# Performance work log

Measured on AMD Instinct MI355X. Metric: run time of the kernel, lower is better.

## Reference

```python
import jax, jax.numpy as jnp
import numpy as np
from jax import lax

N_QUBITS = 12
N_LAYERS = 5
DIM = 2 ** N_QUBITS
EPS = 1e-5


def _linear(x, W, b):
    return x @ W.T + b


def _bn(x, g, b):
    # BatchNorm1d in training mode: biased batch statistics
    mu = jnp.mean(x, axis=0)
    var = jnp.var(x, axis=0)
    return g * (x - mu) * lax.rsqrt(var + EPS) + b


def _leaky(x):
    return jax.nn.leaky_relu(x, 0.01)


def _gate_matrices(w):
    # w: (L, Q, 3) -> composite U3 @ RZ @ RY @ RX per (layer, qubit): (L, Q, 2, 2) complex64
    a, b, c = w[..., 0], w[..., 1], w[..., 2]
    ca = jnp.cos(a / 2).astype(jnp.complex64)
    sa = jnp.sin(a / 2).astype(jnp.complex64)
    cb = jnp.cos(b / 2).astype(jnp.complex64)
    sb = jnp.sin(b / 2).astype(jnp.complex64)
    zero = jnp.zeros_like(ca)

    def mat(m00, m01, m10, m11):
        return jnp.stack([jnp.stack([m00, m01], -1), jnp.stack([m10, m11], -1)], -2)

    RX = mat(ca, -1j * sa, -1j * sa, ca)
    RY = mat(cb, -sb, sb, cb)
    ez = jnp.exp(-0.5j * c.astype(jnp.complex64))
    RZ = mat(ez, zero, zero, jnp.conj(ez))
    eip = jnp.exp(1j * b.astype(jnp.complex64))
    eid = jnp.exp(1j * c.astype(jnp.complex64))
    U3 = mat(ca, -eid * sa, eip * sa, eip * eid * ca)  # pennylane U3(theta=a, phi=b, delta=c)
    mm = lambda A, B: jnp.einsum('lqab,lqbc->lqac', A, B)
    return mm(U3, mm(RZ, mm(RY, RX)))


def _apply1q(state, U, w):
    # state: (B, 2, ..., 2); U: (2, 2) shared across batch
    s = jnp.moveaxis(state, 1 + w, -1)
    s = jnp.einsum('...a,ca->...c', s, U)
    return jnp.moveaxis(s, -1, 1 + w)


def _cnot(state, c, t):
    s = jnp.moveaxis(state, (1 + c, 1 + t), (-2, -1))
    s = jnp.stack([s[..., 0, :], s[..., 1, ::-1]], axis=-2)
    return jnp.moveaxis(s, (-2, -1), (1 + c, 1 + t))


def _quantum(x_pre, qw):
    # Batched statevector simulation of the pennylane circuit. x_pre: (B, 12)
    B = x_pre.shape[0]
    half = x_pre * (jnp.pi / 2)  # RY(x*pi) from |0> -> [cos(x*pi/2), sin(x*pi/2)]
    vec = jnp.stack([jnp.cos(half), jnp.sin(half)], axis=-1).astype(jnp.complex64)  # (B, Q, 2)
    state = vec[:, 0]
    for q in range(1, N_QUBITS):
        state = jnp.einsum('b...,bq->b...q', state, vec[:, q])  # (B, 2, ..., 2)
    G = _gate_matrices(qw)
    for l in range(N_LAYERS):
        for q in range(N_QUBITS):
            state = _apply1q(state, G[l, q], q)
        if l % 2 == 0:
            for q in range(N_QUBITS - 1):
                state = _cnot(state, q, q + 1)
            state = _cnot(state, N_QUBITS - 1, 0)
        else:
            for q in range(0, N_QUBITS, 2):
                state = _cnot(state, q, (q + N_QUBITS // 2) % N_QUBITS)
    probs = jnp.abs(state.reshape(B, DIM)) ** 2
    idx = np.arange(DIM)
    bits = (idx[None, :] >> (N_QUBITS - 1 - np.arange(N_QUBITS))[:, None]) & 1  # (Q, DIM)
    zsigns = jnp.asarray(1.0 - 2.0 * bits, dtype=jnp.float32)
    zvals = probs @ zsigns.T  # (B, Q) PauliZ expectations
    xvals = []
    for q in range(N_QUBITS // 2):  # PauliX expectations on first Q/2 wires
        s = jnp.moveaxis(state, 1 + q, -1).reshape(B, DIM // 2, 2)
        xvals.append(2.0 * jnp.sum(jnp.real(jnp.conj(s[..., 0]) * s[..., 1]), axis=1))
    return jnp.concatenate([zvals, jnp.stack(xvals, axis=1)], axis=1)  # (B, 18)


def setup_inputs():
    key = jax.random.key(0)
    ks = jax.random.split(key, 16)
    B, NF = 4096, 64

    def W(k, o, i):
        return jax.random.normal(k, (o, i), jnp.float32) * (1.0 / np.sqrt(i))

    z = lambda n: jnp.zeros((n,), jnp.float32)
    o = lambda n: jnp.ones((n,), jnp.float32)
    return {
        'x': jax.random.normal(ks[0], (B, NF), jnp.float32),
        'Ws': W(ks[1], 128, NF), 'bs': z(128),
        'W1': W(ks[2], 256, NF), 'b1': z(256), 'g1': o(256), 'be1': z(256),
        'W2': W(ks[3], 128, 256), 'b2': z(128), 'g2': o(128), 'be2': z(128),
        'W3': W(ks[4], 64, 128), 'b3': z(64), 'g3': o(64), 'be3': z(64),
        'Wp': W(ks[5], N_QUBITS, 64), 'bp': z(N_QUBITS),
        'qw': jax.random.normal(ks[6], (N_LAYERS, N_QUBITS, 3), jnp.float32) * 0.1,
        'Wq1': W(ks[7], 128, 18), 'bq1': z(128), 'gq1': o(128), 'beq1': z(128),
        'Wq2': W(ks[8], 64, 128), 'bq2': z(64), 'gq2': o(64), 'beq2': z(64),
        'Wo1': W(ks[9], 32, 64), 'bo1': z(32),
        'Wo2': W(ks[10], 1, 32), 'bo2': z(1),
    }


def reference(x, Ws, bs, W1, b1, g1, be1, W2, b2, g2, be2, W3, b3, g3, be3,
              Wp, bp, qw, Wq1, bq1, gq1, beq1, Wq2, bq2, gq2, beq2,
              Wo1, bo1, Wo2, bo2):
    skip = _linear(x, Ws, bs)
    x1 = _leaky(_bn(_linear(x, W1, b1), g1, be1))          # dropout is eval-mode identity
    x2 = _leaky(_bn(_linear(x1, W2, b2), g2, be2))
    x3 = _leaky(_bn(_linear(x2, W3, b3), g3, be3)) + 0.1 * x1[:, :64]
    x_pre = jnp.tanh(_linear(x3, Wp, bp))
    q_out = lax.stop_gradient(_quantum(x_pre, qw))         # torch detaches the quantum path
    p1 = _leaky(_bn(_linear(q_out, Wq1, bq1), gq1, beq1)) + skip
    p2 = _leaky(_bn(_linear(p1, Wq2, bq2), gq2, beq2))
    return _linear(_leaky(_linear(p2, Wo1, bo1)), Wo2, bo2)  # (B, 1)
```

## Files before the change

### kernel.cpp

```cpp
#include <hip/hip_runtime.h>
#include <math.h>

#define LEAKY(v) ((v) > 0.f ? (v) : 0.01f * (v))

typedef float f2v __attribute__((ext_vector_type(2)));

__device__ __forceinline__ void cmm2(const float* Ar, const float* Ai,
                                     const float* Br, const float* Bi,
                                     float* Cr, float* Ci) {
#pragma unroll
  for (int r = 0; r < 2; r++)
#pragma unroll
    for (int c = 0; c < 2; c++) {
      float xr = 0.f, xi = 0.f;
#pragma unroll
      for (int k = 0; k < 2; k++) {
        float ar = Ar[r*2+k], ai = Ai[r*2+k];
        float br = Br[k*2+c], bi = Bi[k*2+c];
        xr += ar*br - ai*bi;
        xi += ar*bi + ai*br;
      }
      Cr[r*2+c] = xr; Ci[r*2+c] = xi;
    }
}

__global__ __launch_bounds__(256) void prep_k(const float* __restrict__ qw,
                                              float* __restrict__ gates,
                                              float* __restrict__ stats) {
  int t = threadIdx.x;
  for (int i = t; i < 1280; i += 256) stats[i] = 0.f;
  if (t < 60) {
    float a = qw[t*3+0], b = qw[t*3+1], c = qw[t*3+2];
    float ca = cosf(0.5f*a), sa = sinf(0.5f*a);
    float cb = cosf(0.5f*b), sb = sinf(0.5f*b);
    float RXr[4] = {ca, 0.f, 0.f, ca};
    float RXi[4] = {0.f, -sa, -sa, 0.f};
    float RYr[4] = {cb, -sb, sb, cb};
    float RYi[4] = {0.f, 0.f, 0.f, 0.f};
    float hc = 0.5f*c;
    float RZr[4] = {cosf(hc), 0.f, 0.f, cosf(hc)};
    float RZi[4] = {-sinf(hc), 0.f, 0.f, sinf(hc)};
    float epr = cosf(b), epi = sinf(b);
    float edr = cosf(c), edi = sinf(c);
    float eer = epr*edr - epi*edi, eei = epr*edi + epi*edr;
    float U3r[4] = {ca, -edr*sa, epr*sa, eer*ca};
    float U3i[4] = {0.f, -edi*sa, epi*sa, eei*ca};
    float T1r[4],T1i[4],T2r[4],T2i[4],Gr[4],Gi[4];
    cmm2(RYr,RYi, RXr,RXi, T1r,T1i);
    cmm2(RZr,RZi, T1r,T1i, T2r,T2i);
    cmm2(U3r,U3i, T2r,T2i, Gr,Gi);
#pragma unroll
    for (int m = 0; m < 4; m++) {
      gates[t*8 + 2*m]     = Gr[m];
      gates[t*8 + 2*m + 1] = Gi[m];
    }
  }
}

__global__ __launch_bounds__(256) void gemm_f(
    const float* __restrict__ A1, const float* __restrict__ st1,
    const float* __restrict__ g1, const float* __restrict__ be1, int ld1,
    const float* __restrict__ A2, const float* __restrict__ st2,
    const float* __restrict__ g2, const float* __restrict__ be2, int ld2,
    float scale2,
    const float* __restrict__ W, const float* __restrict__ bias,
    float* __restrict__ C, float* __restrict__ statsOut, int N, int K) {
  __shared__ float As[64][65];
  __shared__ float Bs[64][65];
  __shared__ float sc1[256], sh1[256];
  __shared__ float sc2[128], sh2[128];
  const int r0 = blockIdx.x * 64;
  const int c0 = blockIdx.y * 64;
  const int tid = threadIdx.x;
  const int ty = tid >> 4, tx = tid & 15;
  const bool lk1 = (st1 != nullptr);
  const bool lk2 = (st2 != nullptr);
  for (int k = tid; k < K; k += 256) {
    if (lk1) {
      float mean = st1[2*k] * (1.f/4096.f);
      float var  = st1[2*k+1] * (1.f/4096.f) - mean*mean;
      float s = g1[k] * rsqrtf(var + 1e-5f);
      sc1[k] = s; sh1[k] = be1[k] - mean*s;
    } else { sc1[k] = 1.f; sh1[k] = 0.f; }
    if (A2 && k < 128) {
      if (lk2) {
        float mean = st2[2*k] * (1.f/4096.f);
        float var  = st2[2*k+1] * (1.f/4096.f) - mean*mean;
        float s = g2[k] * rsqrtf(var + 1e-5f);
        sc2[k] = s; sh2[k] = be2[k] - mean*s;
      } else { sc2[k] = 1.f; sh2[k] = 0.f; }
    }
  }
  __syncthreads();
  float acc[4][4] = {};
  for (int kc = 0; kc < K; kc += 64) {
#pragma unroll
    for (int i = 0; i < 16; i++) {
      int t = tid + 256*i;
      int lr = t >> 6, lk = t & 63;
      float av = 0.f, wv = 0.f;
      int k = kc + lk;
      if (k < K) {
        float v1 = A1[(size_t)(r0+lr)*ld1 + k];
        v1 = sc1[k]*v1 + sh1[k];
        if (lk1) v1 = LEAKY(v1);
        av = v1;
        if (A2) {
          float v2 = A2[(size_t)(r0+lr)*ld2 + k];
          v2 = sc2[k]*v2 + sh2[k];
          if (lk2) v2 = LEAKY(v2);
          av += scale2 * v2;
        }
        if (c0 + lr < N) wv = W[(size_t)(c0+lr)*K + k];
      }
      As[lr][lk] = av;
      Bs[lr][lk] = wv;
    }
    __syncthreads();
#pragma unroll 16
    for (int kk = 0; kk < 64; kk++) {
      float ar[4], wr[4];
#pragma unroll
      for (int i = 0; i < 4; i++) ar[i] = As[ty*4+i][kk];
#pragma unroll
      for (int j = 0; j < 4; j++) wr[j] = Bs[tx*4+j][kk];
#pragma unroll
      for (int i = 0; i < 4; i++)
#pragma unroll
        for (int j = 0; j < 4; j++)
          acc[i][j] = fmaf(ar[i], wr[j], acc[i][j]);
    }
    __syncthreads();
  }
  float bv[4];
#pragma unroll
  for (int j = 0; j < 4; j++) {
    int c = c0 + tx*4 + j;
    bv[j] = (c < N) ? bias[c] : 0.f;
  }
#pragma unroll
  for (int i = 0; i < 4; i++) {
    int r = r0 + ty*4 + i;
#pragma unroll
    for (int j = 0; j < 4; j++) {
      int c = c0 + tx*4 + j;
      if (c < N) C[(size_t)r*N + c] = acc[i][j] + bv[j];
    }
  }
  if (statsOut) {
    __syncthreads();
#pragma unroll
    for (int j = 0; j < 4; j++) {
      float s = 0.f, q = 0.f;
#pragma unroll
      for (int i = 0; i < 4; i++) {
        float v = acc[i][j] + bv[j];
        s += v; q += v*v;
      }
      As[ty][tx*4+j] = s;
      Bs[ty][tx*4+j] = q;
    }
    __syncthreads();
    if (tid < 64) {
      float s = 0.f, q = 0.f;
#pragma unroll
      for (int t = 0; t < 16; t++) { s += As[t][tid]; q += Bs[t][tid]; }
      int c = c0 + tid;
      if (c < N) {
        atomicAdd(&statsOut[2*c], s);
        atomicAdd(&statsOut[2*c+1], q);
      }
    }
  }
}

__device__ __forceinline__ int SWZi(int i) { return i ^ ((i >> 4) & 15); }
__device__ __forceinline__ int LINV_E(int i) {
  return i ^ ((i >> 1) & 0x7FF) ^ ((i & 1) ? 0xC00 : 0);
}
__device__ __forceinline__ int LINV_O(int i) {
  int hi = i & 0xAAA;
  return (i & 0x555) | ((hi ^ (hi << 6)) & 0xA80) | ((hi >> 6) & 0x2A);
}

template<int B>
__device__ __forceinline__ void gate16(f2v* a, const float* __restrict__ g) {
  const float g00r=g[0], g00i=g[1], g01r=g[2], g01i=g[3];
  const float g10r=g[4], g10i=g[5], g11r=g[6], g11i=g[7];
#pragma unroll
  for (int m = 0; m < 8; m++) {
    const int l0 = ((m >> B) << (B+1)) | (m & ((1<<B)-1));
    const int l1 = l0 | (1 << B);
    f2v A = a[l0], Bv = a[l1];
    f2v Ai; Ai.x = -A.y;  Ai.y = A.x;
    f2v Bi; Bi.x = -Bv.y; Bi.y = Bv.x;
    a[l0] = g00r*A + (g00i*Ai + (g01r*Bv + g01i*Bi));
    a[l1] = g10r*A + (g10i*Ai + (g11r*Bv + g11i*Bi));
  }
}

__global__ __launch_bounds__(256, 4) void quantum_k(const float* __restrict__ zpre,
                                                    const float* __restrict__ gates,
                                                    float* __restrict__ qout) {
  __shared__ f2v st[4096];
  float* stf = (float*)st;
  const int tid = threadIdx.x, b = blockIdx.x;
  if (tid < 12) {
    float xp = tanhf(zpre[b*12 + tid]);
    float h = xp * 1.57079632679489662f;
    stf[tid] = cosf(h);
    stf[12 + tid] = sinf(h);
  }
  __syncthreads();
  float cs[12], sn[12];
#pragma unroll
  for (int q = 0; q < 12; q++) { cs[q] = stf[q]; sn[q] = stf[12+q]; }
  __syncthreads();
  f2v a[16];
  {
    float pre = 1.f;
#pragma unroll
    for (int q = 0; q < 8; q++) pre *= ((tid >> (7-q)) & 1) ? sn[q] : cs[q];
#pragma unroll
    for (int l = 0; l < 16; l++) {
      float v = pre;
      v *= (l & 8) ? sn[8]  : cs[8];
      v *= (l & 4) ? sn[9]  : cs[9];
      v *= (l & 2) ? sn[10] : cs[10];
      v *= (l & 1) ? sn[11] : cs[11];
      a[l].x = v; a[l].y = 0.f;
    }
  }
  const int mA    = tid & 15;
  const int baseA = (tid << 4) | mA;
  const int baseB = ((tid >> 4) << 8) | mA;
  const int baseC = tid ^ ((tid >> 4) & 15);
  const int gE    = SWZi(LINV_E(tid << 4));
  const int gO    = SWZi(LINV_O(tid << 4));
  for (int layer = 0; layer < 5; layer++) {
    const float* gl = gates + layer * 96;
    gate16<3>(a, gl + 64); gate16<2>(a, gl + 72);
    gate16<1>(a, gl + 80); gate16<0>(a, gl + 88);
#pragma unroll
    for (int l = 0; l < 16; l++) st[baseA ^ l] = a[l];
    __syncthreads();
#pragma unroll
    for (int l = 0; l < 16; l++) a[l] = st[baseB ^ ((l << 4) | l)];
    gate16<3>(a, gl + 32); gate16<2>(a, gl + 40);
    gate16<1>(a, gl + 48); gate16<0>(a, gl + 56);
#pragma unroll
    for (int l = 0; l < 16; l++) st[baseB ^ ((l << 4) | l)] = a[l];
    __syncthreads();
#pragma unroll
    for (int l = 0; l < 16; l++) a[l] = st[baseC ^ (l << 8)];
    gate16<3>(a, gl +  0); gate16<2>(a, gl +  8);
    gate16<1>(a, gl + 16); gate16<0>(a, gl + 24);
#pragma unroll
    for (int l = 0; l < 16; l++) st[baseC ^ (l << 8)] = a[l];
    __syncthreads();
    if ((layer & 1) == 0) {
#pragma unroll
      for (int l = 0; l < 16; l++) a[l] = st[gE ^ SWZi(LINV_E(l))];
    } else {
#pragma unroll
      for (int l = 0; l < 16; l++) a[l] = st[gO ^ SWZi(LINV_O(l))];
    }
    __syncthreads();
  }
#pragma unroll
  for (int l = 0; l < 16; l++) st[baseA ^ l] = a[l];
  __syncthreads();
  float pl[16], tot = 0.f;
#pragma unroll
  for (int l = 0; l < 16; l++) { pl[l] = a[l].x*a[l].x + a[l].y*a[l].y; tot += pl[l]; }
  float part[18];
#pragma unroll
  for (int q = 0; q < 8; q++) part[q] = ((tid >> (7-q)) & 1) ? -tot : tot;
#pragma unroll
  for (int q = 8; q < 12; q++) {
    const int bit = 11 - q;
    float s = 0.f;
#pragma unroll
    for (int l = 0; l < 16; l++) s += ((l >> bit) & 1) ? -pl[l] : pl[l];
    part[q] = s;
  }
#pragma unroll
  for (int q = 0; q < 6; q++) {
    const int bt = 7 - q;
    float s = 0.f;
    if (((tid >> bt) & 1) == 0) {
      const int tid2 = tid | (1 << bt);
      const int baseA2 = (tid2 << 4) | (tid2 & 15);
#pragma unroll
      for (int l = 0; l < 16; l++) {
        f2v bb = st[baseA2 ^ l];
        s += a[l].x*bb.x + a[l].y*bb.y;
      }
    }
    part[12+q] = 2.f * s;
  }
  __syncthreads();
#pragma unroll
  for (int j = 0; j < 18; j++) {
    float v = part[j];
#pragma unroll
    for (int m = 1; m < 64; m <<= 1) v += __shfl_xor(v, m);
    if ((tid & 63) == 0) stf[(tid >> 6)*18 + j] = v;
  }
  __syncthreads();
  if (tid < 18) qout[b*18 + tid] = stf[tid] + stf[18+tid] + stf[36+tid] + stf[54+tid];
}

__global__ __launch_bounds__(256) void final_k(const float* __restrict__ P2,
                                               const float* __restrict__ stats,
                                               const float* __restrict__ g,
                                               const float* __restrict__ be,
                                               const float* __restrict__ Wo1,
                                               const float* __restrict__ bo1,
                                               const float* __restrict__ Wo2,
                                               const float* __restrict__ bo2,
                                               float* __restrict__ out) {
  __shared__ float sc[64], sh[64];
  int tid = threadIdx.x;
  if (tid < 64) {
    float mean = stats[2*tid] * (1.f/4096.f);
    float var  = stats[2*tid+1] * (1.f/4096.f) - mean*mean;
    float s = g[tid] * rsqrtf(var + 1e-5f);
    sc[tid] = s; sh[tid] = be[tid] - mean*s;
  }
  __syncthreads();
  int row = blockIdx.x*8 + (tid >> 5);
  int o = tid & 31;
  float acc = 0.f;
#pragma unroll 8
  for (int k = 0; k < 64; k++) {
    float v = sc[k]*P2[(size_t)row*64 + k] + sh[k];
    v = LEAKY(v);
    acc = fmaf(v, Wo1[o*64 + k], acc);
  }
  float h = acc + bo1[o];
  h = LEAKY(h);
  float v = h * Wo2[o];
#pragma unroll
  for (int m = 1; m < 32; m <<= 1) v += __shfl_xor(v, m);
  if (o == 0) out[row] = v + bo2[0];
}

extern "C" void kernel_launch(void* const* d_in, const int* in_sizes, int n_in,
                              void* d_out, int out_size, void* d_ws, size_t ws_size,
                              hipStream_t stream) {
  (void)in_sizes; (void)n_in; (void)out_size; (void)ws_size;
  const float* x   = (const float*)d_in[0];
  const float* Wsk = (const float*)d_in[1];
  const float* bs  = (const float*)d_in[2];
  const float* W1  = (const float*)d_in[3];
  const float* b1  = (const float*)d_in[4];
  const float* g1  = (const float*)d_in[5];
  const float* be1 = (const float*)d_in[6];
  const float* W2  = (const float*)d_in[7];
  const float* b2  = (const float*)d_in[8];
  const float* g2  = (const float*)d_in[9];
  const float* be2 = (const float*)d_in[10];
  const float* W3  = (const float*)d_in[11];
  const float* b3  = (const float*)d_in[12];
  const float* g3  = (const float*)d_in[13];
  const float* be3 = (const float*)d_in[14];
  const float* Wp  = (const float*)d_in[15];
  const float* bp  = (const float*)d_in[16];
  const float* qw  = (const float*)d_in[17];
  const float* Wq1 = (const float*)d_in[18];
  const float* bq1 = (const float*)d_in[19];
  const float* gq1 = (const float*)d_in[20];
  const float* beq1= (const float*)d_in[21];
  const float* Wq2 = (const float*)d_in[22];
  const float* bq2 = (const float*)d_in[23];
  const float* gq2 = (const float*)d_in[24];
  const float* beq2= (const float*)d_in[25];
  const float* Wo1 = (const float*)d_in[26];
  const float* bo1 = (const float*)d_in[27];
  const float* Wo2 = (const float*)d_in[28];
  const float* bo2 = (const float*)d_in[29];
  float* out = (float*)d_out;
  float* ws = (float*)d_ws;

  float* GATES = ws;
  float* ST1 = ws + 480;
  float* ST2 = ST1 + 512;
  float* ST3 = ST2 + 256;
  float* SQ1 = ST3 + 128;
  float* SQ2 = SQ1 + 256;
  float* SKIP = ws + 2048;
  float* BUF1 = SKIP + 4096*128;
  float* BUF2 = BUF1 + 4096*256;
  float* BUF3 = BUF2 + 4096*128;
  float* ZP   = BUF3 + 4096*64;
  float* QOUT = ZP + 4096*12;

  dim3 blk(256);
  prep_k<<<1, blk, 0, stream>>>(qw, GATES, ST1);
  gemm_f<<<dim3(64,2), blk, 0, stream>>>(x, nullptr,nullptr,nullptr, 64,
      nullptr,nullptr,nullptr,nullptr, 0, 0.f, Wsk, bs, SKIP, nullptr, 128, 64);
  gemm_f<<<dim3(64,4), blk, 0, stream>>>(x, nullptr,nullptr,nullptr, 64,
      nullptr,nullptr,nullptr,nullptr, 0, 0.f, W1, b1, BUF1, ST1, 256, 64);
  gemm_f<<<dim3(64,2), blk, 0, stream>>>(BUF1, ST1, g1, be1, 256,
      nullptr,nullptr,nullptr,nullptr, 0, 0.f, W2, b2, BUF2, ST2, 128, 256);
  gemm_f<<<dim3(64,1), blk, 0, stream>>>(BUF2, ST2, g2, be2, 128,
      nullptr,nullptr,nullptr,nullptr, 0, 0.f, W3, b3, BUF3, ST3, 64, 128);
  gemm_f<<<dim3(64,1), blk, 0, stream>>>(BUF3, ST3, g3, be3, 64,
      BUF1, ST1, g1, be1, 256, 0.1f, Wp, bp, ZP, nullptr, 12, 64);
  quantum_k<<<dim3(4096), blk, 0, stream>>>(ZP, GATES, QOUT);
  gemm_f<<<dim3(64,2), blk, 0, stream>>>(QOUT, nullptr,nullptr,nullptr, 18,
      nullptr,nullptr,nullptr,nullptr, 0, 0.f, Wq1, bq1, BUF2, SQ1, 128, 18);
  gemm_f<<<dim3(64,1), blk, 0, stream>>>(BUF2, SQ1, gq1, beq1, 128,
      SKIP, nullptr, nullptr, nullptr, 128, 1.0f, Wq2, bq2, BUF3, SQ2, 64, 128);
  final_k<<<dim3(512), blk, 0, stream>>>(BUF3, SQ2, gq2, beq2, Wo1, bo1, Wo2, bo2, out);
}
```

Before: 491.5 us.

## Fuse MLP GEMM chains into persistent kernels with software grid barriers

```diff
diff --git a/kernel.cpp b/kernel.cpp
--- a/kernel.cpp
+++ b/kernel.cpp
@@ -4,6 +4,24 @@
 #define LEAKY(v) ((v) > 0.f ? (v) : 0.01f * (v))
 
 typedef float f2v __attribute__((ext_vector_type(2)));
+
+__device__ __forceinline__ void gridbar(unsigned* cnt, unsigned* gen, unsigned nb) {
+  __syncthreads();
+  if (threadIdx.x == 0) {
+    __threadfence();
+    unsigned g = __hip_atomic_load(gen, __ATOMIC_ACQUIRE, __HIP_MEMORY_SCOPE_AGENT);
+    unsigned a = __hip_atomic_fetch_add(cnt, 1u, __ATOMIC_ACQ_REL, __HIP_MEMORY_SCOPE_AGENT) + 1;
+    if (a == nb) {
+      __hip_atomic_store(cnt, 0u, __ATOMIC_RELAXED, __HIP_MEMORY_SCOPE_AGENT);
+      __hip_atomic_store(gen, g + 1u, __ATOMIC_RELEASE, __HIP_MEMORY_SCOPE_AGENT);
+    } else {
+      int guard = 1 << 20;
+      while (__hip_atomic_load(gen, __ATOMIC_ACQUIRE, __HIP_MEMORY_SCOPE_AGENT) == g && --guard) {}
+    }
+    __threadfence();
+  }
+  __syncthreads();
+}
 
 __device__ __forceinline__ void cmm2(const float* Ar, const float* Ai,
                                      const float* Br, const float* Bi,
@@ -28,7 +46,7 @@
                                               float* __restrict__ gates,
                                               float* __restrict__ stats) {
   int t = threadIdx.x;
-  for (int i = t; i < 1280; i += 256) stats[i] = 0.f;
+  for (int i = t; i < 1288; i += 256) stats[i] = 0.f;
   if (t < 60) {
     float a = qw[t*3+0], b = qw[t*3+1], c = qw[t*3+2];
     float ca = cosf(0.5f*a), sa = sinf(0.5f*a);
@@ -57,7 +75,15 @@
   }
 }
 
-__global__ __launch_bounds__(256) void gemm_f(
+struct GemmLds {
+  float As[64][65];
+  float Bs[64][65];
+  float sc1[256], sh1[256];
+  float sc2[128], sh2[128];
+};
+
+__device__ __forceinline__ void gemm_tile(
+    GemmLds& L, int bx, int by,
     const float* __restrict__ A1, const float* __restrict__ st1,
     const float* __restrict__ g1, const float* __restrict__ be1, int ld1,
     const float* __restrict__ A2, const float* __restrict__ st2,
@@ -65,12 +91,8 @@
     float scale2,
     const float* __restrict__ W, const float* __restrict__ bias,
     float* __restrict__ C, float* __restrict__ statsOut, int N, int K) {
-  __shared__ float As[64][65];
-  __shared__ float Bs[64][65];
-  __shared__ float sc1[256], sh1[256];
-  __shared__ float sc2[128], sh2[128];
-  const int r0 = blockIdx.x * 64;
-  const int c0 = blockIdx.y * 64;
+  const int r0 = bx * 64;
+  const int c0 = by * 64;
   const int tid = threadIdx.x;
   const int ty = tid >> 4, tx = tid & 15;
   const bool lk1 = (st1 != nullptr);
@@ -80,15 +102,15 @@
       float mean = st1[2*k] * (1.f/4096.f);
       float var  = st1[2*k+1] * (1.f/4096.f) - mean*mean;
       float s = g1[k] * rsqrtf(var + 1e-5f);
-      sc1[k] = s; sh1[k] = be1[k] - mean*s;
-    } else { sc1[k] = 1.f; sh1[k] = 0.f; }
+      L.sc1[k] = s; L.sh1[k] = be1[k] - mean*s;
+    } else { L.sc1[k] = 1.f; L.sh1[k] = 0.f; }
     if (A2 && k < 128) {
       if (lk2) {
         float mean = st2[2*k] * (1.f/4096.f);
         float var  = st2[2*k+1] * (1.f/4096.f) - mean*mean;
         float s = g2[k] * rsqrtf(var + 1e-5f);
-        sc2[k] = s; sh2[k] = be2[k] - mean*s;
-      } else { sc2[k] = 1.f; sh2[k] = 0.f; }
+        L.sc2[k] = s; L.sh2[k] = be2[k] - mean*s;
+      } else { L.sc2[k] = 1.f; L.sh2[k] = 0.f; }
     }
   }
   __syncthreads();
@@ -102,28 +124,28 @@
       int k = kc + lk;
       if (k < K) {
         float v1 = A1[(size_t)(r0+lr)*ld1 + k];
-        v1 = sc1[k]*v1 + sh1[k];
+        v1 = L.sc1[k]*v1 + L.sh1[k];
         if (lk1) v1 = LEAKY(v1);
         av = v1;
         if (A2) {
           float v2 = A2[(size_t)(r0+lr)*ld2 + k];
-          v2 = sc2[k]*v2 + sh2[k];
+          v2 = L.sc2[k]*v2 + L.sh2[k];
           if (lk2) v2 = LEAKY(v2);
           av += scale2 * v2;
         }
         if (c0 + lr < N) wv = W[(size_t)(c0+lr)*K + k];
       }
-      As[lr][lk] = av;
-      Bs[lr][lk] = wv;
+      L.As[lr][lk] = av;
+      L.Bs[lr][lk] = wv;
     }
     __syncthreads();
 #pragma unroll 16
     for (int kk = 0; kk < 64; kk++) {
       float ar[4], wr[4];
 #pragma unroll
-      for (int i = 0; i < 4; i++) ar[i] = As[ty*4+i][kk];
-#pragma unroll
-      for (int j = 0; j < 4; j++) wr[j] = Bs[tx*4+j][kk];
+      for (int i = 0; i < 4; i++) ar[i] = L.As[ty*4+i][kk];
+#pragma unroll
+      for (int j = 0; j < 4; j++) wr[j] = L.Bs[tx*4+j][kk];
 #pragma unroll
       for (int i = 0; i < 4; i++)
 #pragma unroll
@@ -157,21 +179,61 @@
         float v = acc[i][j] + bv[j];
         s += v; q += v*v;
       }
-      As[ty][tx*4+j] = s;
-      Bs[ty][tx*4+j] = q;
+      L.As[ty][tx*4+j] = s;
+      L.Bs[ty][tx*4+j] = q;
     }
     __syncthreads();
     if (tid < 64) {
       float s = 0.f, q = 0.f;
 #pragma unroll
-      for (int t = 0; t < 16; t++) { s += As[t][tid]; q += Bs[t][tid]; }
+      for (int t = 0; t < 16; t++) { s += L.As[t][tid]; q += L.Bs[t][tid]; }
       int c = c0 + tid;
       if (c < N) {
         atomicAdd(&statsOut[2*c], s);
         atomicAdd(&statsOut[2*c+1], q);
       }
     }
-  }
+    __syncthreads();
+  }
+}
+
+struct PreArgs {
+  const float *x, *Wsk, *bs, *W1, *b1, *g1, *be1, *W2, *b2, *g2, *be2,
+              *W3, *b3, *g3, *be3, *Wp, *bp;
+  float *STATS, *SKIP, *BUF1, *BUF2, *BUF3, *ZP;
+  unsigned *SYNC;
+};
+
+__global__ __launch_bounds__(256) void fused_pre(PreArgs p) {
+  __shared__ GemmLds L;
+  const int bid = blockIdx.x;
+  unsigned* cnt = p.SYNC;
+  unsigned* gen = p.SYNC + 1;
+  if (bid < 256)
+    gemm_tile(L, bid % 64, bid / 64, p.x, nullptr,nullptr,nullptr, 64,
+              nullptr,nullptr,nullptr,nullptr, 0, 0.f,
+              p.W1, p.b1, p.BUF1, p.STATS, 256, 64);
+  else {
+    int js = bid - 256;
+    gemm_tile(L, js % 64, js / 64, p.x, nullptr,nullptr,nullptr, 64,
+              nullptr,nullptr,nullptr,nullptr, 0, 0.f,
+              p.Wsk, p.bs, p.SKIP, nullptr, 128, 64);
+  }
+  gridbar(cnt, gen, 384);
+  if (bid < 128)
+    gemm_tile(L, bid % 64, bid / 64, p.BUF1, p.STATS, p.g1, p.be1, 256,
+              nullptr,nullptr,nullptr,nullptr, 0, 0.f,
+              p.W2, p.b2, p.BUF2, p.STATS + 512, 128, 256);
+  gridbar(cnt, gen, 384);
+  if (bid < 64)
+    gemm_tile(L, bid, 0, p.BUF2, p.STATS + 512, p.g2, p.be2, 128,
+              nullptr,nullptr,nullptr,nullptr, 0, 0.f,
+              p.W3, p.b3, p.BUF3, p.STATS + 768, 64, 128);
+  gridbar(cnt, gen, 384);
+  if (bid < 64)
+    gemm_tile(L, bid, 0, p.BUF3, p.STATS + 768, p.g3, p.be3, 64,
+              p.BUF1, p.STATS, p.g1, p.be1, 256, 0.1f,
+              p.Wp, p.bp, p.ZP, nullptr, 12, 64);
 }
 
 __device__ __forceinline__ int SWZi(int i) { return i ^ ((i >> 4) & 15); }
@@ -311,39 +373,54 @@
   if (tid < 18) qout[b*18 + tid] = stf[tid] + stf[18+tid] + stf[36+tid] + stf[54+tid];
 }
 
-__global__ __launch_bounds__(256) void final_k(const float* __restrict__ P2,
-                                               const float* __restrict__ stats,
-                                               const float* __restrict__ g,
-                                               const float* __restrict__ be,
-                                               const float* __restrict__ Wo1,
-                                               const float* __restrict__ bo1,
-                                               const float* __restrict__ Wo2,
-                                               const float* __restrict__ bo2,
-                                               float* __restrict__ out) {
-  __shared__ float sc[64], sh[64];
-  int tid = threadIdx.x;
+struct PostArgs {
+  const float *QOUT, *Wq1, *bq1, *gq1, *beq1, *Wq2, *bq2, *gq2, *beq2,
+              *SKIP, *Wo1, *bo1, *Wo2, *bo2;
+  float *STATS, *BUF2, *BUF3, *out;
+  unsigned *SYNC;
+};
+
+__global__ __launch_bounds__(256) void fused_post(PostArgs p) {
+  __shared__ GemmLds L;
+  const int bid = blockIdx.x, tid = threadIdx.x;
+  unsigned* cnt = p.SYNC;
+  unsigned* gen = p.SYNC + 1;
+  if (bid < 128)
+    gemm_tile(L, bid % 64, bid / 64, p.QOUT, nullptr,nullptr,nullptr, 18,
+              nullptr,nullptr,nullptr,nullptr, 0, 0.f,
+              p.Wq1, p.bq1, p.BUF2, p.STATS + 896, 128, 18);
+  gridbar(cnt, gen, 256);
+  if (bid < 64)
+    gemm_tile(L, bid, 0, p.BUF2, p.STATS + 896, p.gq1, p.beq1, 128,
+              p.SKIP, nullptr, nullptr, nullptr, 128, 1.0f,
+              p.Wq2, p.bq2, p.BUF3, p.STATS + 1152, 64, 128);
+  gridbar(cnt, gen, 256);
   if (tid < 64) {
-    float mean = stats[2*tid] * (1.f/4096.f);
-    float var  = stats[2*tid+1] * (1.f/4096.f) - mean*mean;
-    float s = g[tid] * rsqrtf(var + 1e-5f);
-    sc[tid] = s; sh[tid] = be[tid] - mean*s;
-  }
-  __syncthreads();
-  int row = blockIdx.x*8 + (tid >> 5);
-  int o = tid & 31;
-  float acc = 0.f;
+    const float* SQ2 = p.STATS + 1152;
+    float mean = SQ2[2*tid] * (1.f/4096.f);
+    float var  = SQ2[2*tid+1] * (1.f/4096.f) - mean*mean;
+    float s = p.gq2[tid] * rsqrtf(var + 1e-5f);
+    L.sc2[tid] = s; L.sh2[tid] = p.beq2[tid] - mean*s;
+  }
+  __syncthreads();
+#pragma unroll
+  for (int rr = 0; rr < 2; rr++) {
+    int row = bid*16 + rr*8 + (tid >> 5);
+    int o = tid & 31;
+    float acc = 0.f;
 #pragma unroll 8
-  for (int k = 0; k < 64; k++) {
-    float v = sc[k]*P2[(size_t)row*64 + k] + sh[k];
-    v = LEAKY(v);
-    acc = fmaf(v, Wo1[o*64 + k], acc);
-  }
-  float h = acc + bo1[o];
-  h = LEAKY(h);
-  float v = h * Wo2[o];
-#pragma unroll
-  for (int m = 1; m < 32; m <<= 1) v += __shfl_xor(v, m);
-  if (o == 0) out[row] = v + bo2[0];
+    for (int k = 0; k < 64; k++) {
+      float v = L.sc2[k]*p.BUF3[(size_t)row*64 + k] + L.sh2[k];
+      v = LEAKY(v);
+      acc = fmaf(v, p.Wo1[o*64 + k], acc);
+    }
+    float h = acc + p.bo1[o];
+    h = LEAKY(h);
+    float v = h * p.Wo2[o];
+#pragma unroll
+    for (int m = 1; m < 32; m <<= 1) v += __shfl_xor(v, m);
+    if (o == 0) p.out[row] = v + p.bo2[0];
+  }
 }
 
 extern "C" void kernel_launch(void* const* d_in, const int* in_sizes, int n_in,
@@ -384,11 +461,8 @@
   float* ws = (float*)d_ws;
 
   float* GATES = ws;
-  float* ST1 = ws + 480;
-  float* ST2 = ST1 + 512;
-  float* ST3 = ST2 + 256;
-  float* SQ1 = ST3 + 128;
-  float* SQ2 = SQ1 + 256;
+  float* STATS = ws + 480;
+  unsigned* SYNC = (unsigned*)(ws + 1760);
   float* SKIP = ws + 2048;
   float* BUF1 = SKIP + 4096*128;
   float* BUF2 = BUF1 + 4096*256;
@@ -396,22 +470,17 @@
   float* ZP   = BUF3 + 4096*64;
   float* QOUT = ZP + 4096*12;
 
-  dim3 blk(256);
-  prep_k<<<1, blk, 0, stream>>>(qw, GATES, ST1);
-  gemm_f<<<dim3(64,2), blk, 0, stream>>>(x, nullptr,nullptr,nullptr, 64,
-      nullptr,nullptr,nullptr,nullptr, 0, 0.f, Wsk, bs, SKIP, nullptr, 128, 64);
-  gemm_f<<<dim3(64,4), blk, 0, stream>>>(x, nullptr,nullptr,nullptr, 64,
-      nullptr,nullptr,nullptr,nullptr, 0, 0.f, W1, b1, BUF1, ST1, 256, 64);
-  gemm_f<<<dim3(64,2), blk, 0, stream>>>(BUF1, ST1, g1, be1, 256,
-      nullptr,nullptr,nullptr,nullptr, 0, 0.f, W2, b2, BUF2, ST2, 128, 256);
-  gemm_f<<<dim3(64,1), blk, 0, stream>>>(BUF2, ST2, g2, be2, 128,
-      nullptr,nullptr,nullptr,nullptr, 0, 0.f, W3, b3, BUF3, ST3, 64, 128);
-  gemm_f<<<dim3(64,1), blk, 0, stream>>>(BUF3, ST3, g3, be3, 64,
-      BUF1, ST1, g1, be1, 256, 0.1f, Wp, bp, ZP, nullptr, 12, 64);
-  quantum_k<<<dim3(4096), blk, 0, stream>>>(ZP, GATES, QOUT);
-  gemm_f<<<dim3(64,2), blk, 0, stream>>>(QOUT, nullptr,nullptr,nullptr, 18,
-      nullptr,nullptr,nullptr,nullptr, 0, 0.f, Wq1, bq1, BUF2, SQ1, 128, 18);
-  gemm_f<<<dim3(64,1), blk, 0, stream>>>(BUF2, SQ1, gq1, beq1, 128,
-      SKIP, nullptr, nullptr, nullptr, 128, 1.0f, Wq2, bq2, BUF3, SQ2, 64, 128);
-  final_k<<<dim3(512), blk, 0, stream>>>(BUF3, SQ2, gq2, beq2, Wo1, bo1, Wo2, bo2, out);
-}
+  prep_k<<<1, dim3(256), 0, stream>>>(qw, GATES, STATS);
+
+  PreArgs pa = { x, Wsk, bs, W1, b1, g1, be1, W2, b2, g2, be2,
+                 W3, b3, g3, be3, Wp, bp,
+                 STATS, SKIP, BUF1, BUF2, BUF3, ZP, SYNC };
+  fused_pre<<<dim3(384), dim3(256), 0, stream>>>(pa);
+
+  quantum_k<<<dim3(4096), dim3(256), 0, stream>>>(ZP, GATES, QOUT);
+
+  PostArgs qa = { QOUT, Wq1, bq1, gq1, beq1, Wq2, bq2, gq2, beq2,
+                  SKIP, Wo1, bo1, Wo2, bo2,
+                  STATS, BUF2, BUF3, out, SYNC };
+  fused_post<<<dim3(256), dim3(256), 0, stream>>>(qa);
+}
```

After: 890.2 us. +81.1%, slower.

## Halve GEMM row tile and prefetch next K-chunk into registers

Applied to the files above, without the earlier changes.

```diff
diff --git a/kernel.cpp b/kernel.cpp
--- a/kernel.cpp
+++ b/kernel.cpp
@@ -57,6 +57,45 @@
   }
 }
 
+__device__ __forceinline__ void load_chunk(
+    int tid, int r0, int c0, int kc, int K, int N,
+    const float* __restrict__ A1, int ld1,
+    const float* __restrict__ A2, int ld2, float scale2,
+    bool lk1, bool lk2, const float* __restrict__ W,
+    const float* sc1, const float* sh1,
+    const float* sc2, const float* sh2,
+    float* pa, float* pw) {
+#pragma unroll
+  for (int i = 0; i < 8; i++) {
+    int t = tid + 256*i;
+    int lr = t >> 6, lk = t & 63;
+    int k = kc + lk;
+    float av = 0.f;
+    if (k < K) {
+      float v1 = A1[(size_t)(r0+lr)*ld1 + k];
+      v1 = sc1[k]*v1 + sh1[k];
+      if (lk1) v1 = LEAKY(v1);
+      av = v1;
+      if (A2) {
+        float v2 = A2[(size_t)(r0+lr)*ld2 + k];
+        v2 = sc2[k]*v2 + sh2[k];
+        if (lk2) v2 = LEAKY(v2);
+        av += scale2 * v2;
+      }
+    }
+    pa[i] = av;
+  }
+#pragma unroll
+  for (int i = 0; i < 16; i++) {
+    int t = tid + 256*i;
+    int lr = t >> 6, lk = t & 63;
+    int k = kc + lk;
+    float wv = 0.f;
+    if (k < K && c0 + lr < N) wv = W[(size_t)(c0+lr)*K + k];
+    pw[i] = wv;
+  }
+}
+
 __global__ __launch_bounds__(256) void gemm_f(
     const float* __restrict__ A1, const float* __restrict__ st1,
     const float* __restrict__ g1, const float* __restrict__ be1, int ld1,
@@ -65,11 +104,11 @@
     float scale2,
     const float* __restrict__ W, const float* __restrict__ bias,
     float* __restrict__ C, float* __restrict__ statsOut, int N, int K) {
-  __shared__ float As[64][65];
+  __shared__ float As[32][65];
   __shared__ float Bs[64][65];
   __shared__ float sc1[256], sh1[256];
   __shared__ float sc2[128], sh2[128];
-  const int r0 = blockIdx.x * 64;
+  const int r0 = blockIdx.x * 32;
   const int c0 = blockIdx.y * 64;
   const int tid = threadIdx.x;
   const int ty = tid >> 4, tx = tid & 15;
@@ -92,40 +131,28 @@
     }
   }
   __syncthreads();
-  float acc[4][4] = {};
+  float acc[2][4] = {};
+  float pa[8], pw[16];
+  load_chunk(tid, r0, c0, 0, K, N, A1, ld1, A2, ld2, scale2,
+             lk1, lk2, W, sc1, sh1, sc2, sh2, pa, pw);
   for (int kc = 0; kc < K; kc += 64) {
 #pragma unroll
-    for (int i = 0; i < 16; i++) {
-      int t = tid + 256*i;
-      int lr = t >> 6, lk = t & 63;
-      float av = 0.f, wv = 0.f;
-      int k = kc + lk;
-      if (k < K) {
-        float v1 = A1[(size_t)(r0+lr)*ld1 + k];
-        v1 = sc1[k]*v1 + sh1[k];
-        if (lk1) v1 = LEAKY(v1);
-        av = v1;
-        if (A2) {
-          float v2 = A2[(size_t)(r0+lr)*ld2 + k];
-          v2 = sc2[k]*v2 + sh2[k];
-          if (lk2) v2 = LEAKY(v2);
-          av += scale2 * v2;
-        }
-        if (c0 + lr < N) wv = W[(size_t)(c0+lr)*K + k];
-      }
-      As[lr][lk] = av;
-      Bs[lr][lk] = wv;
-    }
-    __syncthreads();
+    for (int i = 0; i < 8; i++)  { int t = tid + 256*i; As[t>>6][t&63] = pa[i]; }
+#pragma unroll
+    for (int i = 0; i < 16; i++) { int t = tid + 256*i; Bs[t>>6][t&63] = pw[i]; }
+    __syncthreads();
+    if (kc + 64 < K)
+      load_chunk(tid, r0, c0, kc + 64, K, N, A1, ld1, A2, ld2, scale2,
+                 lk1, lk2, W, sc1, sh1, sc2, sh2, pa, pw);
 #pragma unroll 16
     for (int kk = 0; kk < 64; kk++) {
-      float ar[4], wr[4];
-#pragma unroll
-      for (int i = 0; i < 4; i++) ar[i] = As[ty*4+i][kk];
+      float ar[2], wr[4];
+      ar[0] = As[ty*2][kk];
+      ar[1] = As[ty*2+1][kk];
 #pragma unroll
       for (int j = 0; j < 4; j++) wr[j] = Bs[tx*4+j][kk];
 #pragma unroll
-      for (int i = 0; i < 4; i++)
+      for (int i = 0; i < 2; i++)
 #pragma unroll
         for (int j = 0; j < 4; j++)
           acc[i][j] = fmaf(ar[i], wr[j], acc[i][j]);
@@ -139,8 +166,8 @@
     bv[j] = (c < N) ? bias[c] : 0.f;
   }
 #pragma unroll
-  for (int i = 0; i < 4; i++) {
-    int r = r0 + ty*4 + i;
+  for (int i = 0; i < 2; i++) {
+    int r = r0 + ty*2 + i;
 #pragma unroll
     for (int j = 0; j < 4; j++) {
       int c = c0 + tx*4 + j;
@@ -148,12 +175,11 @@
     }
   }
   if (statsOut) {
-    __syncthreads();
 #pragma unroll
     for (int j = 0; j < 4; j++) {
       float s = 0.f, q = 0.f;
 #pragma unroll
-      for (int i = 0; i < 4; i++) {
+      for (int i = 0; i < 2; i++) {
         float v = acc[i][j] + bv[j];
         s += v; q += v*v;
       }
@@ -398,20 +424,20 @@
 
   dim3 blk(256);
   prep_k<<<1, blk, 0, stream>>>(qw, GATES, ST1);
-  gemm_f<<<dim3(64,2), blk, 0, stream>>>(x, nullptr,nullptr,nullptr, 64,
+  gemm_f<<<dim3(128,2), blk, 0, stream>>>(x, nullptr,nullptr,nullptr, 64,
       nullptr,nullptr,nullptr,nullptr, 0, 0.f, Wsk, bs, SKIP, nullptr, 128, 64);
-  gemm_f<<<dim3(64,4), blk, 0, stream>>>(x, nullptr,nullptr,nullptr, 64,
+  gemm_f<<<dim3(128,4), blk, 0, stream>>>(x, nullptr,nullptr,nullptr, 64,
       nullptr,nullptr,nullptr,nullptr, 0, 0.f, W1, b1, BUF1, ST1, 256, 64);
-  gemm_f<<<dim3(64,2), blk, 0, stream>>>(BUF1, ST1, g1, be1, 256,
+  gemm_f<<<dim3(128,2), blk, 0, stream>>>(BUF1, ST1, g1, be1, 256,
       nullptr,nullptr,nullptr,nullptr, 0, 0.f, W2, b2, BUF2, ST2, 128, 256);
-  gemm_f<<<dim3(64,1), blk, 0, stream>>>(BUF2, ST2, g2, be2, 128,
+  gemm_f<<<dim3(128,1), blk, 0, stream>>>(BUF2, ST2, g2, be2, 128,
       nullptr,nullptr,nullptr,nullptr, 0, 0.f, W3, b3, BUF3, ST3, 64, 128);
-  gemm_f<<<dim3(64,1), blk, 0, stream>>>(BUF3, ST3, g3, be3, 64,
+  gemm_f<<<dim3(128,1), blk, 0, stream>>>(BUF3, ST3, g3, be3, 64,
       BUF1, ST1, g1, be1, 256, 0.1f, Wp, bp, ZP, nullptr, 12, 64);
   quantum_k<<<dim3(4096), blk, 0, stream>>>(ZP, GATES, QOUT);
-  gemm_f<<<dim3(64,2), blk, 0, stream>>>(QOUT, nullptr,nullptr,nullptr, 18,
+  gemm_f<<<dim3(128,2), blk, 0, stream>>>(QOUT, nullptr,nullptr,nullptr, 18,
       nullptr,nullptr,nullptr,nullptr, 0, 0.f, Wq1, bq1, BUF2, SQ1, 128, 18);
-  gemm_f<<<dim3(64,1), blk, 0, stream>>>(BUF2, SQ1, gq1, beq1, 128,
+  gemm_f<<<dim3(128,1), blk, 0, stream>>>(BUF2, SQ1, gq1, beq1, 128,
       SKIP, nullptr, nullptr, nullptr, 128, 1.0f, Wq2, bq2, BUF3, SQ2, 64, 128);
   final_k<<<dim3(512), blk, 0, stream>>>(BUF3, SQ2, gq2, beq2, Wo1, bo1, Wo2, bo2, out);
 }
```

Result: faster. 446.6 us (-9.1%).
